# Performance work log

Hardware: AMD Instinct MI355X
Metric: run time of the kernel (lower is better)

## Reference

```python
import jax, jax.numpy as jnp
import numpy as np
from jax import lax

B, T = 32, 20
H, E, A, V = 256, 512, 256, 10000
GH, GW, D = 32, 32, 256          # info spatial grid and channel dim
P = GH * GW                      # num_pixels = 1024
IN_FLAT = P * D                  # 262144
REL = 128 * 128                  # 16384
LSTM_IN = E + D + H              # input to gate linears (x = [word, att_feat], then cat h)


def setup_inputs() -> dict:
    key = jax.random.key(0)
    ks = iter(jax.random.split(key, 40))
    def W(shape, scale=0.05):
        return jax.random.normal(next(ks), shape, jnp.float32) * scale
    inp = {}
    inp["info"] = jax.random.normal(next(ks), (B, GH, GW, D), jnp.float32)
    inp["relation"] = jax.random.normal(next(ks), (B, 128, 128), jnp.float32)
    inp["captions"] = jax.random.randint(next(ks), (B, T), 0, V)
    lens = jax.random.randint(next(ks), (B, 1), 5, T + 1).at[0, 0].set(T)
    inp["captions_lens"] = lens
    # embedding + attention
    inp["emb"] = W((V, E), 0.1)
    inp["W_enc"] = W((D, A)); inp["b_enc"] = jnp.zeros((A,), jnp.float32)
    inp["W_dec"] = W((H, A)); inp["b_dec"] = jnp.zeros((A,), jnp.float32)
    inp["W_full"] = W((A,));  inp["b_full"] = jnp.zeros((), jnp.float32)
    # MSLSTM cell (5 gate linears + mlp)
    for g in ("i", "f", "o", "g1", "g2"):
        inp[f"W_{g}"] = W((LSTM_IN, H)); inp[f"b_{g}"] = jnp.zeros((H,), jnp.float32)
    inp["W_mlp"] = W((2 * H, H)); inp["b_mlp"] = jnp.zeros((H,), jnp.float32)
    # f_beta, fc, init-state linears
    inp["W_beta"] = W((H, D)); inp["b_beta"] = jnp.zeros((D,), jnp.float32)
    inp["W_fc"] = W((H, V), 0.1); inp["b_fc"] = jnp.zeros((V,), jnp.float32)
    inp["W_ih"] = W((IN_FLAT, H), 0.005); inp["b_ih"] = jnp.zeros((H,), jnp.float32)
    inp["W_ic"] = W((IN_FLAT, H), 0.005); inp["b_ic"] = jnp.zeros((H,), jnp.float32)
    inp["W_iC"] = W((REL, H), 0.01);      inp["b_iC"] = jnp.zeros((H,), jnp.float32)
    return inp


def reference(info, relation, captions, captions_lens, emb,
              W_enc, b_enc, W_dec, b_dec, W_full, b_full,
              W_i, b_i, W_f, b_f, W_o, b_o, W_g1, b_g1, W_g2, b_g2,
              W_mlp, b_mlp, W_beta, b_beta, W_fc, b_fc,
              W_ih, b_ih, W_ic, b_ic, W_iC, b_iC):
    Bsz = captions.shape[0]
    info_f = info.reshape(Bsz, P, D)
    rel_f = relation.reshape(Bsz, REL)
    lens = captions_lens[:, 0]
    order = jnp.argsort(-lens)                      # sort descending by length
    lens = lens[order]
    caps = captions[order]
    info_f = info_f[order]
    rel_f = rel_f[order]
    sent_len = lens - 1
    Tm = captions.shape[1] - 1                      # static: max len forced to T in setup

    words = emb[caps]                               # (B, T, E)
    flat = info_f.reshape(Bsz, -1)                  # (B, P*D)
    h = flat @ W_ih + b_ih
    c = flat @ W_ic + b_ic
    C = rel_f @ W_iC + b_iC
    att1 = info_f @ W_enc + b_enc                   # (B, P, A) -- invariant over t

    def step(carry, xs):
        h, c, C = carry
        word, t = xs                                # word: (B, E)
        att2 = h @ W_dec + b_dec                    # (B, A)
        e = jax.nn.relu(att1 + att2[:, None, :]) @ W_full + b_full   # (B, P)
        alpha = jax.nn.softmax(e, axis=1)
        awf = jnp.einsum('bpd,bp->bd', info_f, alpha)                # (B, D)
        # note: gate=sigmoid(f_beta(h)) is computed in torch but its product is unused
        x = jnp.concatenate([word, awf, h], axis=1)  # cat([x, h]) with x=[word, awf]
        i = jax.nn.sigmoid(x @ W_i + b_i)
        f = jax.nn.sigmoid(x @ W_f + b_f)
        o = jax.nn.sigmoid(x @ W_o + b_o)
        g1 = jnp.tanh(x @ W_g1 + b_g1)
        g2 = jnp.tanh(x @ W_g2 + b_g2)
        new_c = f * c + i * g1
        new_C = f * C + i * g2
        new_h = o * jnp.tanh(jnp.concatenate([new_c, new_C], axis=1) @ W_mlp + b_mlp)
        pred = new_h @ W_fc + b_fc                  # dropout in eval mode = identity
        mask = (sent_len > t)[:, None].astype(pred.dtype)
        return (new_h, new_c, new_C), (pred * mask, alpha * mask)

    words_t = jnp.swapaxes(words[:, :Tm], 0, 1)     # (Tm, B, E)
    (_, (preds, alphas)) = lax.scan(step, (h, c, C), (words_t, jnp.arange(Tm)))
    predictions = jnp.swapaxes(preds, 0, 1)         # (B, Tm, V)
    alphas = jnp.swapaxes(alphas, 0, 1)             # (B, Tm, P)
    return predictions, alphas, order
```

## Files before the change

kernel.cpp:

```cpp
#include <hip/hip_runtime.h>
#include <math.h>

#define Bz 32
#define Tz 20
#define TMz 19
#define Vz 10000
#define INFLAT 262144
#define RELSZ 16384
#define NBLK 512

#define WS_PH     0
#define WS_PC     4194304
#define WS_ATT1H  0
#define WS_INFOH  4194304
#define WS_EXPE   8388608
#define WS_ZSUM   8421376
#define WS_AWF    8421888
#define WS_GSP    8430080
#define WS_HST    8593920
#define WS_CST0   8602112
#define WS_CSTB0  8610304
#define WS_CST1   8618496
#define WS_CSTB1  8626688
#define WS_AT2P   8634880
#define WS_INTS   8700416
#define WS_PCHC   8701440
#define WS_WG16   8701440
#define WS_WFC16  9750016
#define WS_END_WFC (9750016 + 1280000)

__device__ __forceinline__ float sigm(float x) { return 1.0f / (1.0f + expf(-x)); }

__device__ __forceinline__ unsigned short f2bf(float f) {
    unsigned int x = __float_as_uint(f);
    unsigned int r = (x + 0x7fffu + ((x >> 16) & 1u)) >> 16;
    return (unsigned short)r;
}
__device__ __forceinline__ float bfl(unsigned int u) { return __uint_as_float(u << 16); }
__device__ __forceinline__ float bfh(unsigned int u) { return __uint_as_float(u & 0xffff0000u); }

__device__ __forceinline__ float agload(const float* p) {
    return __hip_atomic_load(p, __ATOMIC_RELAXED, __HIP_MEMORY_SCOPE_AGENT);
}
__device__ __forceinline__ void agstore(float* p, float v) {
    __hip_atomic_store(p, v, __ATOMIC_RELAXED, __HIP_MEMORY_SCOPE_AGENT);
}
__device__ __forceinline__ int agloadi(const int* p) {
    return __hip_atomic_load(p, __ATOMIC_RELAXED, __HIP_MEMORY_SCOPE_AGENT);
}
__device__ __forceinline__ void agstorei(int* p, int v) {
    __hip_atomic_store(p, v, __ATOMIC_RELAXED, __HIP_MEMORY_SCOPE_AGENT);
}
__device__ __forceinline__ void agadd(float* p, float v) {
    __hip_atomic_fetch_add(p, v, __ATOMIC_RELAXED, __HIP_MEMORY_SCOPE_AGENT);
}

__device__ __forceinline__ void gbar(int* slots, int* root, int gen) {
    asm volatile("s_waitcnt vmcnt(0)" ::: "memory");
    __syncthreads();
    if (blockIdx.x == 0) {
        int i0 = threadIdx.x, i1 = threadIdx.x + 256;
        if (i0 != 0) {
            while (agloadi(&slots[i0]) < gen) __builtin_amdgcn_s_sleep(1);
        }
        while (agloadi(&slots[i1]) < gen) __builtin_amdgcn_s_sleep(1);
        __syncthreads();
        if (threadIdx.x == 0) agstorei(root, gen);
    } else if (threadIdx.x == 0) {
        agstorei(&slots[blockIdx.x], gen);
        while (agloadi(root) < gen) __builtin_amdgcn_s_sleep(2);
    }
    __syncthreads();
    asm volatile("" ::: "memory");
}

__global__ void k_sort(const int* __restrict__ lens, float* __restrict__ out_order,
                       int* __restrict__ ord, int* __restrict__ sentlen, int* __restrict__ barmem) {
    if (threadIdx.x == 0 && blockIdx.x == 0) {
        for (int i = 0; i < 64 + NBLK; ++i) barmem[i] = 0;
        int l[Bz]; bool used[Bz];
        for (int b = 0; b < Bz; ++b) { l[b] = lens[b]; used[b] = false; }
        for (int i = 0; i < Bz; ++i) {
            int best = -1;
            for (int j = 0; j < Bz; ++j)
                if (!used[j] && (best < 0 || l[j] > l[best])) best = j;
            used[best] = true;
            ord[i] = best;
            sentlen[i] = l[best] - 1;
            out_order[i] = (float)best;
        }
    }
}

__global__ __launch_bounds__(256) void k_gemv2(const float* __restrict__ X, const int* __restrict__ ord,
                                               const float* __restrict__ W1, const float* __restrict__ W2,
                                               float* __restrict__ p1, float* __restrict__ p2) {
    __shared__ __align__(16) float xsT[512 * 36];
    __shared__ int ords[32];
    int tid = threadIdx.x;
    size_t k0 = (size_t)blockIdx.x * 512;

    if (tid < 32) ords[tid] = ord[tid];
    __syncthreads();

    for (int idx = tid; idx < 4096; idx += 256) {
        int b = idx >> 7, kq = idx & 127;
        float4 v = *(const float4*)&X[(size_t)ords[b] * INFLAT + k0 + kq * 4];
        xsT[(kq * 4 + 0) * 36 + b] = v.x;
        xsT[(kq * 4 + 1) * 36 + b] = v.y;
        xsT[(kq * 4 + 2) * 36 + b] = v.z;
        xsT[(kq * 4 + 3) * 36 + b] = v.w;
    }
    __syncthreads();

    float ah[32], ac[32];
#pragma unroll
    for (int b = 0; b < 32; ++b) { ah[b] = 0.f; ac[b] = 0.f; }

    const float* w1p = W1 + k0 * 256 + tid;
    const float* w2p = W2 + k0 * 256 + tid;
#pragma unroll 4
    for (int k = 0; k < 512; ++k) {
        float w1 = w1p[(size_t)k * 256];
        float w2 = w2p[(size_t)k * 256];
        const float4* xr = (const float4*)&xsT[k * 36];
#pragma unroll
        for (int bq = 0; bq < 8; ++bq) {
            float4 x4 = xr[bq];
            ah[bq * 4 + 0] += x4.x * w1; ac[bq * 4 + 0] += x4.x * w2;
            ah[bq * 4 + 1] += x4.y * w1; ac[bq * 4 + 1] += x4.y * w2;
            ah[bq * 4 + 2] += x4.z * w1; ac[bq * 4 + 2] += x4.z * w2;
            ah[bq * 4 + 3] += x4.w * w1; ac[bq * 4 + 3] += x4.w * w2;
        }
    }
#pragma unroll
    for (int b = 0; b < 32; ++b) {
        size_t o = ((size_t)blockIdx.x * 32 + b) * 256 + tid;
        p1[o] = ah[b];
        p2[o] = ac[b];
    }
}

__global__ __launch_bounds__(256) void k_gemvC(const float* __restrict__ R, const int* __restrict__ ord,
                                               const float* __restrict__ W, float* __restrict__ p) {
    __shared__ float xs[32 * 128];
    __shared__ int ords[32];
    int tid = threadIdx.x, bx = blockIdx.x;
    if (tid < 32) ords[tid] = ord[tid];
    __syncthreads();
    int k0 = bx * 128;
    for (int idx = tid; idx < 32 * 128; idx += 256) {
        int b = idx >> 7, kk = idx & 127;
        xs[idx] = R[(size_t)ords[b] * RELSZ + k0 + kk];
    }
    __syncthreads();
    float acc[32];
#pragma unroll
    for (int b = 0; b < 32; ++b) acc[b] = 0.f;
    for (int kk = 0; kk < 128; ++kk) {
        float w = W[(size_t)(k0 + kk) * 256 + tid];
#pragma unroll
        for (int b = 0; b < 32; ++b) acc[b] += xs[b * 128 + kk] * w;
    }
#pragma unroll
    for (int b = 0; b < 32; ++b) p[((size_t)bx * 32 + b) * 256 + tid] = acc[b];
}

__global__ __launch_bounds__(256) void k_reduce3(const float* __restrict__ ph, const float* __restrict__ pc,
                                                 const float* __restrict__ pC,
                                                 const float* __restrict__ b_ih, const float* __restrict__ b_ic,
                                                 const float* __restrict__ b_iC,
                                                 float* __restrict__ hst, float* __restrict__ cst,
                                                 float* __restrict__ Cst) {
    int which = blockIdx.x >> 5, b = blockIdx.x & 31, j = threadIdx.x;
    if (which == 0) {
        float s0 = b_ih[j], s1 = 0.f, s2 = 0.f, s3 = 0.f;
        for (int c = 0; c < 512; c += 4) {
            s0 += ph[((size_t)((c + 0) * 32 + b)) * 256 + j];
            s1 += ph[((size_t)((c + 1) * 32 + b)) * 256 + j];
            s2 += ph[((size_t)((c + 2) * 32 + b)) * 256 + j];
            s3 += ph[((size_t)((c + 3) * 32 + b)) * 256 + j];
        }
        hst[b * 256 + j] = s0 + s1 + s2 + s3;
    } else if (which == 1) {
        float s0 = b_ic[j], s1 = 0.f, s2 = 0.f, s3 = 0.f;
        for (int c = 0; c < 512; c += 4) {
            s0 += pc[((size_t)((c + 0) * 32 + b)) * 256 + j];
            s1 += pc[((size_t)((c + 1) * 32 + b)) * 256 + j];
            s2 += pc[((size_t)((c + 2) * 32 + b)) * 256 + j];
            s3 += pc[((size_t)((c + 3) * 32 + b)) * 256 + j];
        }
        cst[b * 256 + j] = s0 + s1 + s2 + s3;
    } else {
        float s0 = b_iC[j], s1 = 0.f, s2 = 0.f, s3 = 0.f;
        for (int c = 0; c < 128; c += 4) {
            s0 += pC[((size_t)((c + 0) * 32 + b)) * 256 + j];
            s1 += pC[((size_t)((c + 1) * 32 + b)) * 256 + j];
            s2 += pC[((size_t)((c + 2) * 32 + b)) * 256 + j];
            s3 += pC[((size_t)((c + 3) * 32 + b)) * 256 + j];
        }
        Cst[b * 256 + j] = s0 + s1 + s2 + s3;
    }
}

__global__ __launch_bounds__(256) void k_init2(const float* __restrict__ hst, const float* __restrict__ W_dec,
                                               float* __restrict__ at2p, float* __restrict__ awf,
                                               float* __restrict__ zsum) {
    __shared__ __align__(16) float hs[8192];
    int tid = threadIdx.x;
    for (int i = blockIdx.x * 256 + tid; i < 8192; i += 1024) awf[i] = 0.f;
    if (blockIdx.x == 0 && tid < 32) zsum[tid] = 0.f;
    for (int i = tid; i < 2048; i += 256) ((float4*)hs)[i] = ((const float4*)hst)[i];
    __syncthreads();
    int col = blockIdx.x * 64 + (tid & 63), bg = tid >> 6;
    float acc[8] = {0.f,0.f,0.f,0.f,0.f,0.f,0.f,0.f};
    for (int k = 0; k < 256; ++k) {
        float w = W_dec[(size_t)k * 256 + col];
#pragma unroll
        for (int bi = 0; bi < 8; ++bi) acc[bi] += hs[(bg * 8 + bi) * 256 + k] * w;
    }
#pragma unroll
    for (int bi = 0; bi < 8; ++bi) {
        int b = bg * 8 + bi;
        at2p[((size_t)(b * 8 + 0)) * 256 + col] = acc[bi];
#pragma unroll
        for (int ct = 1; ct < 8; ++ct) at2p[((size_t)(b * 8 + ct)) * 256 + col] = 0.f;
    }
}

__global__ __launch_bounds__(256) void k_wfc16(const float* __restrict__ W_fc,
                                               unsigned short* __restrict__ wfcT16) {
    __shared__ unsigned short tile[16 * 256];
    int tid = threadIdx.x;
    int c0 = blockIdx.x * 16;
    for (int p = 0; p < 16; ++p) {
        int r = p * 16 + (tid >> 4);
        int c = tid & 15;
        tile[c * 256 + r] = f2bf(W_fc[(size_t)r * Vz + c0 + c]);
    }
    __syncthreads();
    unsigned int* dst = (unsigned int*)wfcT16 + (size_t)c0 * 128;
    const unsigned int* src = (const unsigned int*)tile;
    for (int i = tid; i < 2048; i += 256) dst[i] = src[i];
}

__global__ __launch_bounds__(256) void k_wg16(const float* __restrict__ W_i, const float* __restrict__ W_f,
                                              const float* __restrict__ W_o, const float* __restrict__ W_g1,
                                              const float* __restrict__ W_g2,
                                              unsigned short* __restrict__ wg16) {
    __shared__ unsigned short tile[16 * 1024];
    int tid = threadIdx.x;
    int g = blockIdx.x >> 4;
    int c0 = (blockIdx.x & 15) * 16;
    const float* Wg = (g == 0) ? W_i : (g == 1) ? W_f : (g == 2) ? W_o : (g == 3) ? W_g1 : W_g2;
    for (int p = 0; p < 64; ++p) {
        int r = p * 16 + (tid >> 4);
        int c = tid & 15;
        tile[c * 1024 + r] = f2bf(Wg[(size_t)r * 256 + c0 + c]);
    }
    __syncthreads();
    unsigned int* dst = (unsigned int*)wg16 + ((size_t)(g * 256 + c0)) * 512;
    const unsigned int* src = (const unsigned int*)tile;
    for (int i = tid; i < 8192; i += 256) dst[i] = src[i];
}

__global__ __launch_bounds__(256) void k_att1(const float* __restrict__ info, const int* __restrict__ ord,
                                              const float* __restrict__ W, const float* __restrict__ bias,
                                              unsigned short* __restrict__ att1h,
                                              unsigned short* __restrict__ infoh) {
    __shared__ __align__(16) float xsT[256 * 36];
    int tid = threadIdx.x;
    int r0 = blockIdx.x * 32;
    int b = r0 >> 10, p0 = r0 & 1023;
    const float* src = info + (size_t)ord[b] * INFLAT + (size_t)p0 * 256;
    for (int idx = tid; idx < 2048; idx += 256) {
        int r = idx >> 6, kq = idx & 63;
        float4 v = *(const float4*)&src[r * 256 + kq * 4];
        xsT[(kq * 4 + 0) * 36 + r] = v.x;
        xsT[(kq * 4 + 1) * 36 + r] = v.y;
        xsT[(kq * 4 + 2) * 36 + r] = v.z;
        xsT[(kq * 4 + 3) * 36 + r] = v.w;
    }
    __syncthreads();
#pragma unroll 4
    for (int r = 0; r < 32; ++r)
        infoh[(size_t)(r0 + r) * 256 + tid] = f2bf(xsT[tid * 36 + r]);
    float acc[32];
#pragma unroll
    for (int r = 0; r < 32; ++r) acc[r] = 0.f;
    for (int k = 0; k < 256; ++k) {
        float w = W[k * 256 + tid];
        const float4* xr = (const float4*)&xsT[k * 36];
#pragma unroll
        for (int rq = 0; rq < 8; ++rq) {
            float4 x4 = xr[rq];
            acc[rq * 4 + 0] += x4.x * w;
            acc[rq * 4 + 1] += x4.y * w;
            acc[rq * 4 + 2] += x4.z * w;
            acc[rq * 4 + 3] += x4.w * w;
        }
    }
    float bj = bias[tid];
#pragma unroll
    for (int r = 0; r < 32; ++r)
        att1h[(size_t)(r0 + r) * 256 + tid] = f2bf(acc[r] + bj);
}

struct KArgs {
    const float *info, *emb, *W_dec, *b_dec, *W_full, *b_full;
    const float *b_i, *b_f, *b_o, *b_g1, *b_g2;
    const float *W_mlp, *b_mlp, *W_fc, *b_fc;
    const int *caps;
    const unsigned short *att1h, *infoh, *wfcT16, *wg16;
    float *expe, *zsum, *awf, *gsp, *hst, *cst0, *Cst0, *cst1, *Cst1, *at2p;
    const int *ord, *slp;
    int *root, *slots;
    float *out_pred, *out_alpha;
};

__device__ void pred_task2(const KArgs& a, unsigned short* hb, int tile, int tm1) {
    int tid = threadIdx.x;
    for (int i = tid; i < 8192; i += 256) hb[i] = f2bf(agload(&a.hst[i]));
    __syncthreads();
    int col = tile * 64 + (tid & 63), bg = tid >> 6;
    if (col >= Vz) return;
    float acc[8] = {0.f, 0.f, 0.f, 0.f, 0.f, 0.f, 0.f, 0.f};
    if (a.wfcT16) {
        const uint4* wcol = (const uint4*)(a.wfcT16 + (size_t)col * 256);
#pragma unroll 4
        for (int q = 0; q < 32; ++q) {
            uint4 u = wcol[q];
            float w0 = bfl(u.x), w1 = bfh(u.x), w2 = bfl(u.y), w3 = bfh(u.y);
            float w4 = bfl(u.z), w5 = bfh(u.z), w6 = bfl(u.w), w7 = bfh(u.w);
#pragma unroll
            for (int bi = 0; bi < 8; ++bi) {
                uint4 hv = *(const uint4*)&hb[(bg * 8 + bi) * 256 + q * 8];
                acc[bi] += bfl(hv.x) * w0 + bfh(hv.x) * w1 + bfl(hv.y) * w2 + bfh(hv.y) * w3
                         + bfl(hv.z) * w4 + bfh(hv.z) * w5 + bfl(hv.w) * w6 + bfh(hv.w) * w7;
            }
        }
    } else {
        for (int jq = 0; jq < 64; ++jq) {
            float w0 = a.W_fc[(size_t)(jq * 4 + 0) * Vz + col];
            float w1 = a.W_fc[(size_t)(jq * 4 + 1) * Vz + col];
            float w2 = a.W_fc[(size_t)(jq * 4 + 2) * Vz + col];
            float w3 = a.W_fc[(size_t)(jq * 4 + 3) * Vz + col];
#pragma unroll
            for (int bi = 0; bi < 8; ++bi) {
                uint2 u = *(const uint2*)&hb[(bg * 8 + bi) * 256 + jq * 4];
                acc[bi] += bfl(u.x) * w0 + bfh(u.x) * w1 + bfl(u.y) * w2 + bfh(u.y) * w3;
            }
        }
    }
    float bv = a.b_fc[col];
#pragma unroll
    for (int bi = 0; bi < 8; ++bi) {
        int b = bg * 8 + bi;
        float r = (a.slp[b] > tm1) ? (acc[bi] + bv) : 0.f;
        a.out_pred[((size_t)b * TMz + tm1) * Vz + col] = r;
    }
}

__global__ __launch_bounds__(256, 2) void k_steps(KArgs a) {
    __shared__ __align__(16) unsigned char smem[81920];
    unsigned char* attB = smem;
    unsigned char* infB = smem + 32768;
    float* F = (float*)(smem + 65536);
    unsigned short* S16 = (unsigned short*)(smem + 65536);

    int bid = blockIdx.x, tid = threadIdx.x;
    int b = bid >> 4, sub = bid & 15;
    int gen = 0;

    {
        const unsigned short* ag = a.att1h + (size_t)(b * 1024 + sub * 64) * 256;
        const unsigned short* ig = a.infoh + (size_t)(b * 1024 + sub * 64) * 256;
        for (int idx = tid; idx < 2048; idx += 256) {
            int r = idx >> 5, qc = idx & 31;
            uint4 v = *(const uint4*)(ag + (size_t)r * 256 + qc * 8);
            *(uint4*)(attB + r * 512 + ((qc ^ (r & 7)) << 4)) = v;
            uint4 w2 = *(const uint4*)(ig + (size_t)r * 256 + qc * 8);
            *(uint4*)(infB + idx * 16) = w2;
        }
    }
    __syncthreads();

    for (int t = 0; t < TMz; ++t) {
        {
            float v = a.b_dec[tid];
#pragma unroll
            for (int ct = 0; ct < 8; ++ct) v += agload(&a.at2p[((size_t)(b * 8 + ct)) * 256 + tid]);
            F[tid] = v;
            F[256 + tid] = a.W_full[tid];
            __syncthreads();
            int pl = tid & 63, kq = tid >> 6;
            float part = 0.f;
#pragma unroll
            for (int q = 0; q < 8; ++q) {
                int c = kq * 8 + q;
                uint4 u = *(const uint4*)(attB + pl * 512 + ((c ^ (pl & 7)) << 4));
                const float* A = F + kq * 64 + q * 8;
                const float* W = F + 256 + kq * 64 + q * 8;
                part += fmaxf(bfl(u.x) + A[0], 0.f) * W[0];
                part += fmaxf(bfh(u.x) + A[1], 0.f) * W[1];
                part += fmaxf(bfl(u.y) + A[2], 0.f) * W[2];
                part += fmaxf(bfh(u.y) + A[3], 0.f) * W[3];
                part += fmaxf(bfl(u.z) + A[4], 0.f) * W[4];
                part += fmaxf(bfh(u.z) + A[5], 0.f) * W[5];
                part += fmaxf(bfl(u.w) + A[6], 0.f) * W[6];
                part += fmaxf(bfh(u.w) + A[7], 0.f) * W[7];
            }
            F[512 + kq * 64 + pl] = part;
            __syncthreads();
            if (tid < 64) {
                float e = F[512 + tid] + F[576 + tid] + F[640 + tid] + F[704 + tid] + a.b_full[0];
                float ex = expf(e);
                agstore(&a.expe[b * 1024 + sub * 64 + tid], ex);
                F[768 + tid] = ex;
                float s = ex;
                s += __shfl_down(s, 32); s += __shfl_down(s, 16); s += __shfl_down(s, 8);
                s += __shfl_down(s, 4);  s += __shfl_down(s, 2);  s += __shfl_down(s, 1);
                if (tid == 0) agadd(&a.zsum[b], s);
            }
            __syncthreads();
            int gg = tid >> 7, c2 = tid & 127;
            const unsigned char* ib = infB + gg * 512 + c2 * 4;
            const float* ex = F + 768;
            float a0 = 0.f, a1 = 0.f;
#pragma unroll
            for (int i = 0; i < 32; ++i) {
                unsigned int u = *(const unsigned int*)(ib + i * 1024);
                float ev = ex[i * 2 + gg];
                a0 += ev * bfl(u);
                a1 += ev * bfh(u);
            }
            F[832 + gg * 256 + c2 * 2]     = a0;
            F[832 + gg * 256 + c2 * 2 + 1] = a1;
            __syncthreads();
            agadd(&a.awf[b * 256 + tid], F[832 + tid] + F[1088 + tid]);
        }
        gbar(a.slots, a.root, ++gen);

        if (bid < 80) {
            int g = bid / 16, s16 = bid % 16;
            int ct = s16 >> 2, kc = s16 & 3;
            for (int idx = tid; idx < 8192; idx += 256) {
                int b2 = idx >> 8, kk = idx & 255;
                float v;
                if (kc == 0) {
                    int cap = a.caps[a.ord[b2] * Tz + t];
                    v = a.emb[(size_t)cap * 512 + kk];
                } else if (kc == 1) {
                    int cap = a.caps[a.ord[b2] * Tz + t];
                    v = a.emb[(size_t)cap * 512 + 256 + kk];
                } else if (kc == 2) {
                    v = agload(&a.awf[b2 * 256 + kk]);
                } else {
                    v = agload(&a.hst[b2 * 256 + kk]);
                }
                S16[idx] = f2bf(v);
            }
            __syncthreads();
            int col = ct * 64 + (tid & 63), bg = tid >> 6;
            const uint4* wcol = (const uint4*)(a.wg16 + ((size_t)(g * 256 + col)) * 1024 + kc * 256);
            float acc[8] = {0.f,0.f,0.f,0.f,0.f,0.f,0.f,0.f};
#pragma unroll 4
            for (int q = 0; q < 32; ++q) {
                uint4 u = wcol[q];
                float w0 = bfl(u.x), w1 = bfh(u.x), w2 = bfl(u.y), w3 = bfh(u.y);
                float w4 = bfl(u.z), w5 = bfh(u.z), w6 = bfl(u.w), w7 = bfh(u.w);
#pragma unroll
                for (int bi = 0; bi < 8; ++bi) {
                    uint4 xv = *(const uint4*)&S16[(bg * 8 + bi) * 256 + q * 8];
                    acc[bi] += bfl(xv.x) * w0 + bfh(xv.x) * w1 + bfl(xv.y) * w2 + bfh(xv.y) * w3
                             + bfl(xv.z) * w4 + bfh(xv.z) * w5 + bfl(xv.w) * w6 + bfh(xv.w) * w7;
                }
            }
            if (kc == 2) {
#pragma unroll
                for (int bi = 0; bi < 8; ++bi) {
                    float Z = agload(&a.zsum[bg * 8 + bi]);
                    acc[bi] *= (1.0f / Z);
                }
            }
#pragma unroll
            for (int bi = 0; bi < 8; ++bi)
                agstore(&a.gsp[((size_t)((g * 4 + kc) * 32 + bg * 8 + bi)) * 256 + col], acc[bi]);
        } else if (bid < 237) {
            if (bid < 112) {
                int bb = bid - 80;
                float Z = agload(&a.zsum[bb]);
                float invZ = 1.0f / Z;
                float am = (a.slp[bb] > t) ? invZ : 0.f;
                float* oal = a.out_alpha + ((size_t)bb * TMz + t) * 1024;
                for (int p = tid; p < 1024; p += 256) oal[p] = agload(&a.expe[bb * 1024 + p]) * am;
            }
            if (t > 0) pred_task2(a, S16, bid - 80, t - 1);
        }
        gbar(a.slots, a.root, ++gen);

        if (bid < 256) {
            int bb = bid >> 3, ct = bid & 7;
            int j = tid;
            const float* csOld = (t & 1) ? a.cst1 : a.cst0;
            const float* CsOld = (t & 1) ? a.Cst1 : a.Cst0;
            float* csNew = (t & 1) ? a.cst0 : a.cst1;
            float* CsNew = (t & 1) ? a.Cst0 : a.Cst1;
            float gs[5];
#pragma unroll
            for (int g = 0; g < 5; ++g) {
                float s = 0.f;
#pragma unroll
                for (int kc = 0; kc < 4; ++kc)
                    s += agload(&a.gsp[((size_t)((g * 4 + kc) * 32 + bb)) * 256 + j]);
                gs[g] = s;
            }
            gs[0] += a.b_i[j]; gs[1] += a.b_f[j]; gs[2] += a.b_o[j];
            gs[3] += a.b_g1[j]; gs[4] += a.b_g2[j];
            float iv = sigm(gs[0]), fv = sigm(gs[1]), ov = sigm(gs[2]);
            float g1 = tanhf(gs[3]), g2 = tanhf(gs[4]);
            float nc = fv * agload(&csOld[bb * 256 + j]) + iv * g1;
            float nC = fv * agload(&CsOld[bb * 256 + j]) + iv * g2;
            if (ct == 0) {
                agstore(&csNew[bb * 256 + j], nc);
                agstore(&CsNew[bb * 256 + j], nC);
            }
            if (ct == 1 && tid == 0) agstore(&a.zsum[bb], 0.f);
            F[j] = nc;
            F[256 + j] = nC;
            F[512 + j] = ov;
            __syncthreads();
            int colL = tid & 31, kth = tid >> 5;
            int col = ct * 32 + colL;
            float part = 0.f;
            const float* wm = a.W_mlp + col;
            for (int i = 0; i < 64; ++i) {
                int k = kth * 64 + i;
                part += F[k] * wm[(size_t)k * 256];
            }
            F[768 + colL * 9 + kth] = part;
            __syncthreads();
            if (tid < 32) {
                int c2 = ct * 32 + tid;
                float m = a.b_mlp[c2];
#pragma unroll
                for (int kk = 0; kk < 8; ++kk) m += F[768 + tid * 9 + kk];
                float hv = F[512 + c2] * tanhf(m);
                agstore(&a.hst[bb * 256 + c2], hv);
                F[1056 + tid] = hv;
                agstore(&a.awf[bb * 256 + c2], 0.f);
            }
            __syncthreads();
            float acc = 0.f;
            const float* wd = a.W_dec + (size_t)(ct * 32) * 256 + tid;
#pragma unroll
            for (int kk = 0; kk < 32; ++kk) acc += F[1056 + kk] * wd[(size_t)kk * 256];
            agstore(&a.at2p[((size_t)(bb * 8 + ct)) * 256 + tid], acc);
        }
        gbar(a.slots, a.root, ++gen);
    }

    if (bid >= 80 && bid < 237) pred_task2(a, S16, bid - 80, TMz - 1);
}

extern "C" void kernel_launch(void* const* d_in, const int* in_sizes, int n_in,
                              void* d_out, int out_size, void* d_ws, size_t ws_size,
                              hipStream_t stream) {
    const float* info  = (const float*)d_in[0];
    const float* rel   = (const float*)d_in[1];
    const int*   caps  = (const int*)d_in[2];
    const int*   lens  = (const int*)d_in[3];
    const float* emb   = (const float*)d_in[4];
    const float* W_enc = (const float*)d_in[5];
    const float* b_enc = (const float*)d_in[6];
    const float* W_dec = (const float*)d_in[7];
    const float* b_dec = (const float*)d_in[8];
    const float* W_full= (const float*)d_in[9];
    const float* b_full= (const float*)d_in[10];
    const float* W_i   = (const float*)d_in[11];
    const float* b_i   = (const float*)d_in[12];
    const float* W_f   = (const float*)d_in[13];
    const float* b_f   = (const float*)d_in[14];
    const float* W_o   = (const float*)d_in[15];
    const float* b_o   = (const float*)d_in[16];
    const float* W_g1  = (const float*)d_in[17];
    const float* b_g1  = (const float*)d_in[18];
    const float* W_g2  = (const float*)d_in[19];
    const float* b_g2  = (const float*)d_in[20];
    const float* W_mlp = (const float*)d_in[21];
    const float* b_mlp = (const float*)d_in[22];
    const float* W_fc  = (const float*)d_in[25];
    const float* b_fc  = (const float*)d_in[26];
    const float* W_ih  = (const float*)d_in[27];
    const float* b_ih  = (const float*)d_in[28];
    const float* W_ic  = (const float*)d_in[29];
    const float* b_ic  = (const float*)d_in[30];
    const float* W_iC  = (const float*)d_in[31];
    const float* b_iC  = (const float*)d_in[32];

    float* out = (float*)d_out;
    float* out_pred  = out;
    float* out_alpha = out + (size_t)Bz * TMz * Vz;
    float* out_order = out_alpha + (size_t)Bz * TMz * 1024;

    float* w = (float*)d_ws;
    float* ph   = w + WS_PH;
    float* pcp  = w + WS_PC;
    unsigned short* att1h = (unsigned short*)(w + WS_ATT1H);
    unsigned short* infoh = (unsigned short*)(w + WS_INFOH);
    float* expe = w + WS_EXPE;
    float* zsum = w + WS_ZSUM;
    float* awf  = w + WS_AWF;
    float* gsp  = w + WS_GSP;
    float* hst  = w + WS_HST;
    float* cst0 = w + WS_CST0;
    float* Cst0 = w + WS_CSTB0;
    float* cst1 = w + WS_CST1;
    float* Cst1 = w + WS_CSTB1;
    float* at2p = w + WS_AT2P;
    int*   ordp = (int*)(w + WS_INTS);
    int*   slp  = ordp + 32;
    int*   barmem = ordp + 64;
    float* pC   = w + WS_PCHC;
    unsigned short* wg16   = (unsigned short*)(w + WS_WG16);
    unsigned short* wfcT16 = (unsigned short*)(w + WS_WFC16);

    int useWfc = (ws_size >= (size_t)WS_END_WFC * 4);

    k_sort<<<1, 64, 0, stream>>>(lens, out_order, ordp, slp, barmem);
    k_gemv2<<<512, 256, 0, stream>>>(info, ordp, W_ih, W_ic, ph, pcp);
    k_gemvC<<<128, 256, 0, stream>>>(rel, ordp, W_iC, pC);
    k_reduce3<<<96, 256, 0, stream>>>(ph, pcp, pC, b_ih, b_ic, b_iC, hst, cst0, Cst0);
    k_init2<<<4, 256, 0, stream>>>(hst, W_dec, at2p, awf, zsum);
    k_wg16<<<80, 256, 0, stream>>>(W_i, W_f, W_o, W_g1, W_g2, wg16);
    if (useWfc) k_wfc16<<<625, 256, 0, stream>>>(W_fc, wfcT16);
    k_att1<<<1024, 256, 0, stream>>>(info, ordp, W_enc, b_enc, att1h, infoh);

    KArgs ka;
    ka.info = info; ka.emb = emb; ka.W_dec = W_dec; ka.b_dec = b_dec;
    ka.W_full = W_full; ka.b_full = b_full;
    ka.b_i = b_i; ka.b_f = b_f; ka.b_o = b_o; ka.b_g1 = b_g1; ka.b_g2 = b_g2;
    ka.W_mlp = W_mlp; ka.b_mlp = b_mlp; ka.W_fc = W_fc; ka.b_fc = b_fc;
    ka.caps = caps;
    ka.att1h = att1h; ka.infoh = infoh;
    ka.wfcT16 = useWfc ? wfcT16 : (const unsigned short*)0;
    ka.wg16 = wg16;
    ka.expe = expe; ka.zsum = zsum; ka.awf = awf;
    ka.gsp = gsp; ka.hst = hst;
    ka.cst0 = cst0; ka.Cst0 = Cst0; ka.cst1 = cst1; ka.Cst1 = Cst1;
    ka.at2p = at2p;
    ka.ord = ordp; ka.slp = slp;
    ka.root = barmem; ka.slots = barmem + 64;
    ka.out_pred = out_pred; ka.out_alpha = out_alpha;

    k_steps<<<NBLK, 256, 0, stream>>>(ka);
}
```

Before: 1.950 ms.

## Fold cell update into attention phase to drop one grid barrier per step

The LSTM cell update, MLP, and W_dec projection now run redundantly in every block at the start of each step. This removes the separate cell phase and its grid-wide barrier, along with the at2p partial-sum buffers. The c/C states stay in registers, and awf/zsum are double-buffered by step parity so they can be zeroed one step ahead without a race. In exchange, each block re-reads W_mlp and W_dec every step, which adds serial per-thread GEMV work and L2 traffic.

Measured after the change: 3.938 ms. +101.9%, slower.

```diff
diff --git a/kernel.cpp b/kernel.cpp
--- a/kernel.cpp
+++ b/kernel.cpp
@@ -14,15 +14,12 @@
 #define WS_ATT1H  0
 #define WS_INFOH  4194304
 #define WS_EXPE   8388608
-#define WS_ZSUM   8421376
-#define WS_AWF    8421888
 #define WS_GSP    8430080
 #define WS_HST    8593920
 #define WS_CST0   8602112
 #define WS_CSTB0  8610304
-#define WS_CST1   8618496
-#define WS_CSTB1  8626688
-#define WS_AT2P   8634880
+#define WS_AWF2   8634880
+#define WS_ZSUM2  8651264
 #define WS_INTS   8700416
 #define WS_PCHC   8701440
 #define WS_WG16   8701440
@@ -203,29 +200,10 @@
     }
 }
 
-__global__ __launch_bounds__(256) void k_init2(const float* __restrict__ hst, const float* __restrict__ W_dec,
-                                               float* __restrict__ at2p, float* __restrict__ awf,
-                                               float* __restrict__ zsum) {
-    __shared__ __align__(16) float hs[8192];
-    int tid = threadIdx.x;
-    for (int i = blockIdx.x * 256 + tid; i < 8192; i += 1024) awf[i] = 0.f;
-    if (blockIdx.x == 0 && tid < 32) zsum[tid] = 0.f;
-    for (int i = tid; i < 2048; i += 256) ((float4*)hs)[i] = ((const float4*)hst)[i];
-    __syncthreads();
-    int col = blockIdx.x * 64 + (tid & 63), bg = tid >> 6;
-    float acc[8] = {0.f,0.f,0.f,0.f,0.f,0.f,0.f,0.f};
-    for (int k = 0; k < 256; ++k) {
-        float w = W_dec[(size_t)k * 256 + col];
-#pragma unroll
-        for (int bi = 0; bi < 8; ++bi) acc[bi] += hs[(bg * 8 + bi) * 256 + k] * w;
-    }
-#pragma unroll
-    for (int bi = 0; bi < 8; ++bi) {
-        int b = bg * 8 + bi;
-        at2p[((size_t)(b * 8 + 0)) * 256 + col] = acc[bi];
-#pragma unroll
-        for (int ct = 1; ct < 8; ++ct) at2p[((size_t)(b * 8 + ct)) * 256 + col] = 0.f;
-    }
+__global__ __launch_bounds__(256) void k_init2(float* __restrict__ awf2, float* __restrict__ zsum2) {
+    int i0 = blockIdx.x * 256 + threadIdx.x;
+    for (int i = i0; i < 16384; i += 1024) awf2[i] = 0.f;
+    if (i0 < 64) zsum2[i0] = 0.f;
 }
 
 __global__ __launch_bounds__(256) void k_wfc16(const float* __restrict__ W_fc,
@@ -307,12 +285,13 @@
 }
 
 struct KArgs {
-    const float *info, *emb, *W_dec, *b_dec, *W_full, *b_full;
+    const float *emb, *W_dec, *b_dec, *W_full, *b_full;
     const float *b_i, *b_f, *b_o, *b_g1, *b_g2;
     const float *W_mlp, *b_mlp, *W_fc, *b_fc;
     const int *caps;
     const unsigned short *att1h, *infoh, *wfcT16, *wg16;
-    float *expe, *zsum, *awf, *gsp, *hst, *cst0, *Cst0, *cst1, *Cst1, *at2p;
+    const float *h0, *c0, *C0;
+    float *expe, *zsum2, *awf2, *gsp, *hst;
     const int *ord, *slp;
     int *root, *slots;
     float *out_pred, *out_alpha;
@@ -361,6 +340,38 @@
     }
 }
 
+__device__ float cell_h(const KArgs& a, float* F, int b, float& cs_r, float& Cs_r) {
+    int tid = threadIdx.x;
+    float gs[5];
+#pragma unroll
+    for (int g = 0; g < 5; ++g) {
+        float s = 0.f;
+#pragma unroll
+        for (int kc = 0; kc < 4; ++kc)
+            s += agload(&a.gsp[((size_t)((g * 4 + kc) * 32 + b)) * 256 + tid]);
+        gs[g] = s;
+    }
+    gs[0] += a.b_i[tid]; gs[1] += a.b_f[tid]; gs[2] += a.b_o[tid];
+    gs[3] += a.b_g1[tid]; gs[4] += a.b_g2[tid];
+    float iv = sigm(gs[0]), fv = sigm(gs[1]), ov = sigm(gs[2]);
+    float g1 = tanhf(gs[3]), g2 = tanhf(gs[4]);
+    cs_r = fv * cs_r + iv * g1;
+    Cs_r = fv * Cs_r + iv * g2;
+    F[tid] = cs_r;
+    F[256 + tid] = Cs_r;
+    __syncthreads();
+    float m0 = a.b_mlp[tid], m1 = 0.f, m2 = 0.f, m3 = 0.f;
+    const float* wm = a.W_mlp + tid;
+    for (int k = 0; k < 512; k += 4) {
+        m0 += F[k + 0] * wm[(size_t)(k + 0) * 256];
+        m1 += F[k + 1] * wm[(size_t)(k + 1) * 256];
+        m2 += F[k + 2] * wm[(size_t)(k + 2) * 256];
+        m3 += F[k + 3] * wm[(size_t)(k + 3) * 256];
+    }
+    __syncthreads();
+    return ov * tanhf((m0 + m1) + (m2 + m3));
+}
+
 __global__ __launch_bounds__(256, 2) void k_steps(KArgs a) {
     __shared__ __align__(16) unsigned char smem[81920];
     unsigned char* attB = smem;
@@ -385,13 +396,34 @@
     }
     __syncthreads();
 
+    float cs_r = a.c0[b * 256 + tid];
+    float Cs_r = a.C0[b * 256 + tid];
+
     for (int t = 0; t < TMz; ++t) {
         {
-            float v = a.b_dec[tid];
-#pragma unroll
-            for (int ct = 0; ct < 8; ++ct) v += agload(&a.at2p[((size_t)(b * 8 + ct)) * 256 + tid]);
-            F[tid] = v;
-            F[256 + tid] = a.W_full[tid];
+            float hv;
+            if (t == 0) {
+                hv = a.h0[b * 256 + tid];
+            } else {
+                hv = cell_h(a, F, b, cs_r, Cs_r);
+            }
+            if (sub == 0) agstore(&a.hst[b * 256 + tid], hv);
+            F[512 + tid] = hv;
+            __syncthreads();
+            {
+                float s0 = a.b_dec[tid], s1 = 0.f, s2 = 0.f, s3 = 0.f;
+                const float* wd = a.W_dec + tid;
+                for (int k = 0; k < 256; k += 4) {
+                    s0 += F[512 + k + 0] * wd[(size_t)(k + 0) * 256];
+                    s1 += F[512 + k + 1] * wd[(size_t)(k + 1) * 256];
+                    s2 += F[512 + k + 2] * wd[(size_t)(k + 2) * 256];
+                    s3 += F[512 + k + 3] * wd[(size_t)(k + 3) * 256];
+                }
+                float at2v = (s0 + s1) + (s2 + s3);
+                __syncthreads();
+                F[tid] = at2v;
+                F[256 + tid] = a.W_full[tid];
+            }
             __syncthreads();
             int pl = tid & 63, kq = tid >> 6;
             float part = 0.f;
@@ -420,7 +452,7 @@
                 float s = ex;
                 s += __shfl_down(s, 32); s += __shfl_down(s, 16); s += __shfl_down(s, 8);
                 s += __shfl_down(s, 4);  s += __shfl_down(s, 2);  s += __shfl_down(s, 1);
-                if (tid == 0) agadd(&a.zsum[b], s);
+                if (tid == 0) agadd(&a.zsum2[(t & 1) * 32 + b], s);
             }
             __syncthreads();
             int gg = tid >> 7, c2 = tid & 127;
@@ -437,7 +469,7 @@
             F[832 + gg * 256 + c2 * 2]     = a0;
             F[832 + gg * 256 + c2 * 2 + 1] = a1;
             __syncthreads();
-            agadd(&a.awf[b * 256 + tid], F[832 + tid] + F[1088 + tid]);
+            agadd(&a.awf2[(t & 1) * 8192 + b * 256 + tid], F[832 + tid] + F[1088 + tid]);
         }
         gbar(a.slots, a.root, ++gen);
 
@@ -454,7 +486,7 @@
                     int cap = a.caps[a.ord[b2] * Tz + t];
                     v = a.emb[(size_t)cap * 512 + 256 + kk];
                 } else if (kc == 2) {
-                    v = agload(&a.awf[b2 * 256 + kk]);
+                    v = agload(&a.awf2[(t & 1) * 8192 + b2 * 256 + kk]);
                 } else {
                     v = agload(&a.hst[b2 * 256 + kk]);
                 }
@@ -479,7 +511,7 @@
             if (kc == 2) {
 #pragma unroll
                 for (int bi = 0; bi < 8; ++bi) {
-                    float Z = agload(&a.zsum[bg * 8 + bi]);
+                    float Z = agload(&a.zsum2[(t & 1) * 32 + bg * 8 + bi]);
                     acc[bi] *= (1.0f / Z);
                 }
             }
@@ -489,77 +521,24 @@
         } else if (bid < 237) {
             if (bid < 112) {
                 int bb = bid - 80;
-                float Z = agload(&a.zsum[bb]);
+                float Z = agload(&a.zsum2[(t & 1) * 32 + bb]);
                 float invZ = 1.0f / Z;
                 float am = (a.slp[bb] > t) ? invZ : 0.f;
                 float* oal = a.out_alpha + ((size_t)bb * TMz + t) * 1024;
                 for (int p = tid; p < 1024; p += 256) oal[p] = agload(&a.expe[bb * 1024 + p]) * am;
+                agstore(&a.awf2[((t + 1) & 1) * 8192 + bb * 256 + tid], 0.f);
+                if (tid == 0) agstore(&a.zsum2[((t + 1) & 1) * 32 + bb], 0.f);
             }
             if (t > 0) pred_task2(a, S16, bid - 80, t - 1);
         }
         gbar(a.slots, a.root, ++gen);
-
-        if (bid < 256) {
-            int bb = bid >> 3, ct = bid & 7;
-            int j = tid;
-            const float* csOld = (t & 1) ? a.cst1 : a.cst0;
-            const float* CsOld = (t & 1) ? a.Cst1 : a.Cst0;
-            float* csNew = (t & 1) ? a.cst0 : a.cst1;
-            float* CsNew = (t & 1) ? a.Cst0 : a.Cst1;
-            float gs[5];
-#pragma unroll
-            for (int g = 0; g < 5; ++g) {
-                float s = 0.f;
-#pragma unroll
-                for (int kc = 0; kc < 4; ++kc)
-                    s += agload(&a.gsp[((size_t)((g * 4 + kc) * 32 + bb)) * 256 + j]);
-                gs[g] = s;
-            }
-            gs[0] += a.b_i[j]; gs[1] += a.b_f[j]; gs[2] += a.b_o[j];
-            gs[3] += a.b_g1[j]; gs[4] += a.b_g2[j];
-            float iv = sigm(gs[0]), fv = sigm(gs[1]), ov = sigm(gs[2]);
-            float g1 = tanhf(gs[3]), g2 = tanhf(gs[4]);
-            float nc = fv * agload(&csOld[bb * 256 + j]) + iv * g1;
-            float nC = fv * agload(&CsOld[bb * 256 + j]) + iv * g2;
-            if (ct == 0) {
-                agstore(&csNew[bb * 256 + j], nc);
-                agstore(&CsNew[bb * 256 + j], nC);
-            }
-            if (ct == 1 && tid == 0) agstore(&a.zsum[bb], 0.f);
-            F[j] = nc;
-            F[256 + j] = nC;
-            F[512 + j] = ov;
-            __syncthreads();
-            int colL = tid & 31, kth = tid >> 5;
-            int col = ct * 32 + colL;
-            float part = 0.f;
-            const float* wm = a.W_mlp + col;
-            for (int i = 0; i < 64; ++i) {
-                int k = kth * 64 + i;
-                part += F[k] * wm[(size_t)k * 256];
-            }
-            F[768 + colL * 9 + kth] = part;
-            __syncthreads();
-            if (tid < 32) {
-                int c2 = ct * 32 + tid;
-                float m = a.b_mlp[c2];
-#pragma unroll
-                for (int kk = 0; kk < 8; ++kk) m += F[768 + tid * 9 + kk];
-                float hv = F[512 + c2] * tanhf(m);
-                agstore(&a.hst[bb * 256 + c2], hv);
-                F[1056 + tid] = hv;
-                agstore(&a.awf[bb * 256 + c2], 0.f);
-            }
-            __syncthreads();
-            float acc = 0.f;
-            const float* wd = a.W_dec + (size_t)(ct * 32) * 256 + tid;
-#pragma unroll
-            for (int kk = 0; kk < 32; ++kk) acc += F[1056 + kk] * wd[(size_t)kk * 256];
-            agstore(&a.at2p[((size_t)(bb * 8 + ct)) * 256 + tid], acc);
-        }
-        gbar(a.slots, a.root, ++gen);
-    }
-
+    }
+
+    {
+        float hv = cell_h(a, F, b, cs_r, Cs_r);
+        if (sub == 0) agstore(&a.hst[b * 256 + tid], hv);
+    }
+    gbar(a.slots, a.root, ++gen);
     if (bid >= 80 && bid < 237) pred_task2(a, S16, bid - 80, TMz - 1);
 }
 
@@ -609,15 +588,12 @@
     unsigned short* att1h = (unsigned short*)(w + WS_ATT1H);
     unsigned short* infoh = (unsigned short*)(w + WS_INFOH);
     float* expe = w + WS_EXPE;
-    float* zsum = w + WS_ZSUM;
-    float* awf  = w + WS_AWF;
     float* gsp  = w + WS_GSP;
     float* hst  = w + WS_HST;
     float* cst0 = w + WS_CST0;
     float* Cst0 = w + WS_CSTB0;
-    float* cst1 = w + WS_CST1;
-    float* Cst1 = w + WS_CSTB1;
-    float* at2p = w + WS_AT2P;
+    float* awf2 = w + WS_AWF2;
+    float* zsum2= w + WS_ZSUM2;
     int*   ordp = (int*)(w + WS_INTS);
     int*   slp  = ordp + 32;
     int*   barmem = ordp + 64;
@@ -631,13 +607,13 @@
     k_gemv2<<<512, 256, 0, stream>>>(info, ordp, W_ih, W_ic, ph, pcp);
     k_gemvC<<<128, 256, 0, stream>>>(rel, ordp, W_iC, pC);
     k_reduce3<<<96, 256, 0, stream>>>(ph, pcp, pC, b_ih, b_ic, b_iC, hst, cst0, Cst0);
-    k_init2<<<4, 256, 0, stream>>>(hst, W_dec, at2p, awf, zsum);
+    k_init2<<<4, 256, 0, stream>>>(awf2, zsum2);
     k_wg16<<<80, 256, 0, stream>>>(W_i, W_f, W_o, W_g1, W_g2, wg16);
     if (useWfc) k_wfc16<<<625, 256, 0, stream>>>(W_fc, wfcT16);
     k_att1<<<1024, 256, 0, stream>>>(info, ordp, W_enc, b_enc, att1h, infoh);
 
     KArgs ka;
-    ka.info = info; ka.emb = emb; ka.W_dec = W_dec; ka.b_dec = b_dec;
+    ka.emb = emb; ka.W_dec = W_dec; ka.b_dec = b_dec;
     ka.W_full = W_full; ka.b_full = b_full;
     ka.b_i = b_i; ka.b_f = b_f; ka.b_o = b_o; ka.b_g1 = b_g1; ka.b_g2 = b_g2;
     ka.W_mlp = W_mlp; ka.b_mlp = b_mlp; ka.W_fc = W_fc; ka.b_fc = b_fc;
@@ -645,10 +621,9 @@
     ka.att1h = att1h; ka.infoh = infoh;
     ka.wfcT16 = useWfc ? wfcT16 : (const unsigned short*)0;
     ka.wg16 = wg16;
-    ka.expe = expe; ka.zsum = zsum; ka.awf = awf;
+    ka.h0 = hst; ka.c0 = cst0; ka.C0 = Cst0;
+    ka.expe = expe; ka.zsum2 = zsum2; ka.awf2 = awf2;
     ka.gsp = gsp; ka.hst = hst;
-    ka.cst0 = cst0; ka.Cst0 = Cst0; ka.cst1 = cst1; ka.Cst1 = Cst1;
-    ka.at2p = at2p;
     ka.ord = ordp; ka.slp = slp;
     ka.root = barmem; ka.slots = barmem + 64;
     ka.out_pred = out_pred; ka.out_alpha = out_alpha;
```
